# Optimization experiments

Hardware: AMD Instinct MI355X
Metric: run time of the kernel (lower is better)

The kernel has to match this reference:

```python
import jax, jax.numpy as jnp
import numpy as np

B, S, D, H = 4, 2048, 1024, 16
HEAD = D // H
DENOM = float(np.sqrt(D))  # NOTE: original divides by sqrt(hidden_size), not sqrt(head_size)


def setup_inputs() -> dict:
    key = jax.random.key(0)
    ks = jax.random.split(key, 5)
    scale = 1.0 / np.sqrt(D)
    return {
        "hidden_state": jax.random.normal(ks[0], (B, S, D), dtype=jnp.float32),
        "attention_mask": jnp.ones((B, S), dtype=jnp.int32),  # unused in forward (faithful to source)
        "w_q": jax.random.normal(ks[1], (D, D), dtype=jnp.float32) * scale,
        "w_k": jax.random.normal(ks[2], (D, D), dtype=jnp.float32) * scale,
        "w_v": jax.random.normal(ks[3], (D, D), dtype=jnp.float32) * scale,
        "w_o": jax.random.normal(ks[4], (D, D), dtype=jnp.float32) * scale,
    }


def _split_heads(x):
    # [B, S, D] -> [B, H, S, head]
    b, s, _ = x.shape
    return x.reshape(b, s, H, HEAD).transpose(0, 2, 1, 3)


def reference(hidden_state, attention_mask, w_q, w_k, w_v, w_o):
    # nn.Linear(bias=False): y = x @ W^T with W of shape [out, in]
    q = _split_heads(hidden_state @ w_q.T)  # [B, H, S, head]
    k = _split_heads(hidden_state @ w_k.T)
    v = _split_heads(hidden_state @ w_v.T)
    qk = jnp.einsum("bhqd,bhkd->bhqk", q, k) / DENOM  # scale = 1/sqrt(hidden_size)
    attn = jax.nn.softmax(qk, axis=-1)  # attention_mask is NOT applied (matches source)
    ctx = jnp.einsum("bhqk,bhkd->bhqd", attn, v)  # [B, H, S, head]
    ctx = ctx.transpose(0, 2, 1, 3).reshape(hidden_state.shape[0], hidden_state.shape[1], D)
    return ctx @ w_o.T
```

## Files before the change

### kernel.cpp

```cpp
#include <hip/hip_runtime.h>
#include <hip/hip_bf16.h>
#include <math.h>

typedef __bf16 bf16x8 __attribute__((ext_vector_type(8)));
typedef __bf16 bf16x2 __attribute__((ext_vector_type(2)));
typedef float f32x4 __attribute__((ext_vector_type(4)));
typedef float f32x16 __attribute__((ext_vector_type(16)));
typedef unsigned u32x2v __attribute__((ext_vector_type(2)));
typedef unsigned u32x4v __attribute__((ext_vector_type(4)));
typedef unsigned short u16;

#define QSCALE 0.04508422002778011f

__device__ __forceinline__ u16 f2b(float f) {
  union { float f; unsigned u; } x; x.f = f;
  unsigned r = x.u + 0x7fffu + ((x.u >> 16) & 1u);
  return (u16)(r >> 16);
}

__device__ __forceinline__ unsigned pkbf(float a, float b) {
  bf16x2 t = { (__bf16)a, (__bf16)b };
  return __builtin_bit_cast(unsigned, t);
}

#define GLOAD_LDS16(g, s)                                                      \
  __builtin_amdgcn_global_load_lds(                                            \
      (__attribute__((address_space(1))) void*)(void*)(g),                     \
      (__attribute__((address_space(3))) void*)(s), 16, 0, 0)

#define VMCNT4 asm volatile("s_waitcnt vmcnt(4)" ::: "memory")
#define VMCNT0 asm volatile("s_waitcnt vmcnt(0)" ::: "memory")
#define SBAR   __builtin_amdgcn_s_barrier()

__global__ void cast_bf16_kernel(const float* __restrict__ in, u16* __restrict__ out,
                                 int n4) {
  int i = blockIdx.x * blockDim.x + threadIdx.x;
  int stride = gridDim.x * blockDim.x;
  for (; i < n4; i += stride) {
    float4 v = ((const float4*)in)[i];
    ushort4 o;
    o.x = f2b(v.x); o.y = f2b(v.y); o.z = f2b(v.z); o.w = f2b(v.w);
    ((ushort4*)out)[i] = o;
  }
}

__global__ void cast_w4_kernel(const float* __restrict__ wq, const float* __restrict__ wk,
                               const float* __restrict__ wv, const float* __restrict__ wo,
                               u16* __restrict__ wqkv, u16* __restrict__ wob) {
  const int w = blockIdx.y;
  const float* src = (w == 0) ? wq : (w == 1) ? wk : (w == 2) ? wv : wo;
  u16* dst = (w < 3) ? wqkv + (size_t)w * 1024 * 1024 : wob;
  const float scale = (w == 0) ? QSCALE : 1.0f;
  const int n4 = 1024 * 1024 / 4;
  int i = blockIdx.x * blockDim.x + threadIdx.x;
  int stride = gridDim.x * blockDim.x;
  for (; i < n4; i += stride) {
    float4 v = ((const float4*)src)[i];
    ushort4 o;
    o.x = f2b(v.x * scale); o.y = f2b(v.y * scale);
    o.z = f2b(v.z * scale); o.w = f2b(v.w * scale);
    ((ushort4*)dst)[i] = o;
  }
}

template <int OUT_MODE>
__global__ __launch_bounds__(256) void gemm_nt(const u16* __restrict__ A,
                                               const u16* __restrict__ B,
                                               void* __restrict__ O0,
                                               u16* __restrict__ Ko,
                                               u16* __restrict__ Vt) {
  __shared__ u16 As[2][128 * 32];
  __shared__ u16 Bs[2][128 * 32];
  const int tid = threadIdx.x;
  const int wid = tid >> 6, lane = tid & 63;
  const int fr = lane & 15, fg = lane >> 4;
  const int wr = wid >> 1, wc = wid & 1;
  const int m0 = blockIdx.y * 128, n0 = blockIdx.x * 128;
  const int K = 1024;

  const int srow = tid >> 2, skc = tid & 3;
  const int srow2 = (tid + 256) >> 2;

#define STAGE_G(t_) do {                                                             \
    const int d_ = (t_) & 1;                                                         \
    GLOAD_LDS16(A + (size_t)(m0 + srow) * K + (t_) * 32 + skc * 8,                   \
                (char*)As[d_] + tid * 16);                                           \
    GLOAD_LDS16(A + (size_t)(m0 + srow2) * K + (t_) * 32 + skc * 8,                  \
                (char*)As[d_] + (tid + 256) * 16);                                   \
    GLOAD_LDS16(B + (size_t)(n0 + srow) * K + (t_) * 32 + skc * 8,                   \
                (char*)Bs[d_] + tid * 16);                                           \
    GLOAD_LDS16(B + (size_t)(n0 + srow2) * K + (t_) * 32 + skc * 8,                  \
                (char*)Bs[d_] + (tid + 256) * 16);                                   \
  } while (0)

  f32x4 acc[4][4] = {};

  STAGE_G(0);
  for (int t = 0; t < 32; ++t) {
    const int d = t & 1;
    if (t < 31) { STAGE_G(t + 1); VMCNT4; }
    else        { VMCNT0; }
    SBAR;

    bf16x8 af[4], bfr[4];
#pragma unroll
    for (int m = 0; m < 4; ++m)
      af[m] = *(const bf16x8*)((const char*)As[d] + (wr * 64 + m * 16 + fr) * 64 + fg * 16);
#pragma unroll
    for (int n = 0; n < 4; ++n)
      bfr[n] = *(const bf16x8*)((const char*)Bs[d] + (wc * 64 + n * 16 + fr) * 64 + fg * 16);
    __builtin_amdgcn_s_setprio(1);
#pragma unroll
    for (int m = 0; m < 4; ++m)
#pragma unroll
      for (int n = 0; n < 4; ++n)
        acc[m][n] = __builtin_amdgcn_mfma_f32_16x16x32_bf16(af[m], bfr[n], acc[m][n], 0, 0, 0);
    __builtin_amdgcn_s_setprio(0);
    SBAR;
  }
#undef STAGE_G

#pragma unroll
  for (int m = 0; m < 4; ++m)
#pragma unroll
    for (int n = 0; n < 4; ++n) {
      int gr = m0 + wr * 64 + m * 16 + fg * 4;
      int gc = n0 + wc * 64 + n * 16 + fr;
      if (OUT_MODE == 0) {
#pragma unroll
        for (int j = 0; j < 4; ++j)
          ((float*)O0)[(size_t)(gr + j) * 1024 + gc] = acc[m][n][j];
      } else {
        const int region = n0 >> 10;
        if (region == 2) {
          int vc = gc - 2048;
          int hh = vc >> 6, dd = vc & 63, bb2 = gr >> 11, s0 = gr & 2047;
          ushort4 o;
          o.x = f2b(acc[m][n][0]); o.y = f2b(acc[m][n][1]);
          o.z = f2b(acc[m][n][2]); o.w = f2b(acc[m][n][3]);
          *(ushort4*)(Vt + (((size_t)bb2 * 16 + hh) * 64 + dd) * 2048 + s0) = o;
        } else {
          u16* dst = (region == 0) ? (u16*)O0 : Ko;
          int cc = gc & 1023;
#pragma unroll
          for (int j = 0; j < 4; ++j)
            dst[(size_t)(gr + j) * 1024 + cc] = f2b(acc[m][n][j]);
        }
      }
    }
}

__global__ __launch_bounds__(256, 2) void attn_fwd(const u16* __restrict__ Q,
                                                   const u16* __restrict__ Kg,
                                                   const u16* __restrict__ Vtg,
                                                   u16* __restrict__ O) {
  __shared__ u16 Ks[2][64 * 64];
  __shared__ u16 Vs[2][64 * 64];
  const int tid = threadIdx.x;
  const int wid = tid >> 6, lane = tid & 63;
  const int lq = lane & 31, hi = lane >> 5;
  const int id = blockIdx.x;
  const int swz = (id & 7) * 64 + (id >> 3);
  const int qb = swz & 7, bh = swz >> 3;
  const int b = bh >> 4, h = bh & 15;
  const size_t tokBase = (size_t)b * 2048 * 1024 + h * 64;
  const size_t vBase = (size_t)bh * 64 * 2048;
  const int q0 = qb * 256 + wid * 64;

  bf16x8 qfA[4], qfB[4];
#pragma unroll
  for (int s = 0; s < 4; ++s) {
    qfA[s] = *(const bf16x8*)(Q + tokBase + (size_t)(q0 + lq) * 1024 + s * 16 + hi * 8);
    qfB[s] = *(const bf16x8*)(Q + tokBase + (size_t)(q0 + 32 + lq) * 1024 + s * 16 + hi * 8);
  }

  f32x16 accA0 = {}, accA1 = {}, accB0 = {}, accB1 = {};
  f32x16 lsvA = {}, lsvB = {};

  const int skey = tid >> 3, sdc = tid & 7;
  const int sdg = sdc ^ (skey & 7);
  const int skey2 = (tid + 256) >> 3;
  const int sdg2 = sdc ^ (skey2 & 7);

#define STAGE(bb_, k0_) do {                                                          \
    GLOAD_LDS16(Kg + tokBase + (size_t)((k0_) + skey) * 1024 + sdg * 8,               \
                (char*)Ks[bb_] + tid * 16);                                           \
    GLOAD_LDS16(Kg + tokBase + (size_t)((k0_) + skey2) * 1024 + sdg2 * 8,             \
                (char*)Ks[bb_] + (tid + 256) * 16);                                   \
    GLOAD_LDS16(Vtg + vBase + (size_t)skey * 2048 + (k0_) + sdg * 8,                  \
                (char*)Vs[bb_] + tid * 16);                                           \
    GLOAD_LDS16(Vtg + vBase + (size_t)skey2 * 2048 + (k0_) + sdg2 * 8,                \
                (char*)Vs[bb_] + (tid + 256) * 16);                                   \
  } while (0)

  STAGE(0, 0);
  for (int t = 0; t < 32; ++t) {
    const int bb = t & 1;
    __syncthreads();
    if (t < 31) STAGE(bb ^ 1, (t + 1) * 64);

    f32x16 svA0 = {}, svA1 = {}, svB0 = {}, svB1 = {};
    __builtin_amdgcn_s_setprio(1);
#pragma unroll
    for (int s = 0; s < 4; ++s) {
      bf16x8 kf0 = *(const bf16x8*)((const char*)Ks[bb] + lq * 128 +
                                    ((s * 32 + hi * 16) ^ ((lq & 7) << 4)));
      bf16x8 kf1 = *(const bf16x8*)((const char*)Ks[bb] + (32 + lq) * 128 +
                                    ((s * 32 + hi * 16) ^ ((lq & 7) << 4)));
      svA0 = __builtin_amdgcn_mfma_f32_32x32x16_bf16(kf0, qfA[s], svA0, 0, 0, 0);
      svB0 = __builtin_amdgcn_mfma_f32_32x32x16_bf16(kf0, qfB[s], svB0, 0, 0, 0);
      svA1 = __builtin_amdgcn_mfma_f32_32x32x16_bf16(kf1, qfA[s], svA1, 0, 0, 0);
      svB1 = __builtin_amdgcn_mfma_f32_32x32x16_bf16(kf1, qfB[s], svB1, 0, 0, 0);
    }
    __builtin_amdgcn_s_setprio(0);

#pragma unroll
    for (int i = 0; i < 16; ++i) svA0[i] = __builtin_amdgcn_exp2f(svA0[i]);
#pragma unroll
    for (int i = 0; i < 16; ++i) svA1[i] = __builtin_amdgcn_exp2f(svA1[i]);
#pragma unroll
    for (int i = 0; i < 16; ++i) svB0[i] = __builtin_amdgcn_exp2f(svB0[i]);
#pragma unroll
    for (int i = 0; i < 16; ++i) svB1[i] = __builtin_amdgcn_exp2f(svB1[i]);
    lsvA += svA0; lsvA += svA1;
    lsvB += svB0; lsvB += svB1;

    bf16x8 paA[4], paB[4];
#pragma unroll
    for (int kb = 0; kb < 2; ++kb) {
#pragma unroll
      for (int hh = 0; hh < 2; ++hh) {
        const int rb = hh * 8;
        {
          const f32x16& pv = kb ? svA1 : svA0;
          unsigned w01 = pkbf(pv[rb + 0], pv[rb + 1]);
          unsigned w23 = pkbf(pv[rb + 2], pv[rb + 3]);
          unsigned w45 = pkbf(pv[rb + 4], pv[rb + 5]);
          unsigned w67 = pkbf(pv[rb + 6], pv[rb + 7]);
          u32x2v ra = __builtin_amdgcn_permlane32_swap(w01, w45, false, false);
          u32x2v rc = __builtin_amdgcn_permlane32_swap(w23, w67, false, false);
          u32x4v fw = { ra[0], rc[0], ra[1], rc[1] };
          paA[kb * 2 + hh] = __builtin_bit_cast(bf16x8, fw);
        }
        {
          const f32x16& pv = kb ? svB1 : svB0;
          unsigned w01 = pkbf(pv[rb + 0], pv[rb + 1]);
          unsigned w23 = pkbf(pv[rb + 2], pv[rb + 3]);
          unsigned w45 = pkbf(pv[rb + 4], pv[rb + 5]);
          unsigned w67 = pkbf(pv[rb + 6], pv[rb + 7]);
          u32x2v ra = __builtin_amdgcn_permlane32_swap(w01, w45, false, false);
          u32x2v rc = __builtin_amdgcn_permlane32_swap(w23, w67, false, false);
          u32x4v fw = { ra[0], rc[0], ra[1], rc[1] };
          paB[kb * 2 + hh] = __builtin_bit_cast(bf16x8, fw);
        }
      }
    }

    __builtin_amdgcn_s_setprio(1);
#pragma unroll
    for (int s = 0; s < 4; ++s) {
      bf16x8 bv0 = *(const bf16x8*)((const char*)Vs[bb] + lq * 128 +
                                    ((s * 32 + hi * 16) ^ ((lq & 7) << 4)));
      bf16x8 bv1 = *(const bf16x8*)((const char*)Vs[bb] + (32 + lq) * 128 +
                                    ((s * 32 + hi * 16) ^ ((lq & 7) << 4)));
      accA0 = __builtin_amdgcn_mfma_f32_32x32x16_bf16(paA[s], bv0, accA0, 0, 0, 0);
      accA1 = __builtin_amdgcn_mfma_f32_32x32x16_bf16(paA[s], bv1, accA1, 0, 0, 0);
      accB0 = __builtin_amdgcn_mfma_f32_32x32x16_bf16(paB[s], bv0, accB0, 0, 0, 0);
      accB1 = __builtin_amdgcn_mfma_f32_32x32x16_bf16(paB[s], bv1, accB1, 0, 0, 0);
    }
    __builtin_amdgcn_s_setprio(0);
  }
#undef STAGE

  float totA = 0.f, totB = 0.f;
#pragma unroll
  for (int i = 0; i < 16; ++i) { totA += lsvA[i]; totB += lsvB[i]; }
  totA += __shfl_xor(totA, 32);
  totB += __shfl_xor(totB, 32);
  const float invA = 1.0f / totA, invB = 1.0f / totB;
#pragma unroll
  for (int r = 0; r < 16; ++r) {
    const int q = (r & 3) + 8 * (r >> 2) + 4 * hi;
    const float ivA = __shfl(invA, q);
    const float ivB = __shfl(invB, q);
    const size_t rowA = (size_t)(b * 2048 + q0 + q) * 1024 + h * 64;
    const size_t rowB = (size_t)(b * 2048 + q0 + 32 + q) * 1024 + h * 64;
    O[rowA + lq]      = f2b(accA0[r] * ivA);
    O[rowA + 32 + lq] = f2b(accA1[r] * ivA);
    O[rowB + lq]      = f2b(accB0[r] * ivB);
    O[rowB + 32 + lq] = f2b(accB1[r] * ivB);
  }
}

extern "C" void kernel_launch(void* const* d_in, const int* in_sizes, int n_in,
                              void* d_out, int out_size, void* d_ws, size_t ws_size,
                              hipStream_t stream) {
  const float* hs = (const float*)d_in[0];
  const float* wq = (const float*)d_in[2];
  const float* wk = (const float*)d_in[3];
  const float* wv = (const float*)d_in[4];
  const float* wo = (const float*)d_in[5];

  const size_t TOK = 8192, DD = 1024;
  u16* hsb  = (u16*)d_ws;
  u16* wqkv = hsb + TOK * DD;
  u16* wob  = wqkv + 3 * DD * DD;
  u16* Qb   = wob + DD * DD;
  u16* Kb   = Qb + TOK * DD;
  u16* Vtg  = Kb + TOK * DD;
  u16* Cb   = Vtg + TOK * DD;

  cast_bf16_kernel<<<2048, 256, 0, stream>>>(hs, hsb, (int)(TOK * DD / 4));
  cast_w4_kernel<<<dim3(128, 4), 256, 0, stream>>>(wq, wk, wv, wo, wqkv, wob);

  gemm_nt<1><<<dim3(24, 64), 256, 0, stream>>>(hsb, wqkv, Qb, Kb, Vtg);

  attn_fwd<<<dim3(512), 256, 0, stream>>>(Qb, Kb, Vtg, Cb);

  gemm_nt<0><<<dim3(8, 64), 256, 0, stream>>>(Cb, wob, d_out, nullptr, nullptr);
}
```

Before: 206.5 us.

## Use K=64 single-buffered GEMM tiles with XOR-swizzled LDS layout

Rewrites both projection GEMMs to stage 64-wide K slices per iteration instead of 32. LDS writes and reads use an XOR swizzle to avoid bank conflicts. The double-buffered prefetch pipeline is replaced by a single buffer with __syncthreads, which halves the barrier count per K but no longer overlaps global loads with MFMA. This trades load/compute overlap for fewer iterations and conflict-free LDS reads.

```diff
diff --git a/kernel.cpp b/kernel.cpp
--- a/kernel.cpp
+++ b/kernel.cpp
@@ -27,10 +27,6 @@
   __builtin_amdgcn_global_load_lds(                                            \
       (__attribute__((address_space(1))) void*)(void*)(g),                     \
       (__attribute__((address_space(3))) void*)(s), 16, 0, 0)
-
-#define VMCNT4 asm volatile("s_waitcnt vmcnt(4)" ::: "memory")
-#define VMCNT0 asm volatile("s_waitcnt vmcnt(0)" ::: "memory")
-#define SBAR   __builtin_amdgcn_s_barrier()
 
 __global__ void cast_bf16_kernel(const float* __restrict__ in, u16* __restrict__ out,
                                  int n4) {
@@ -64,13 +60,13 @@
 }
 
 template <int OUT_MODE>
-__global__ __launch_bounds__(256) void gemm_nt(const u16* __restrict__ A,
-                                               const u16* __restrict__ B,
-                                               void* __restrict__ O0,
-                                               u16* __restrict__ Ko,
-                                               u16* __restrict__ Vt) {
-  __shared__ u16 As[2][128 * 32];
-  __shared__ u16 Bs[2][128 * 32];
+__global__ __launch_bounds__(256) void gemm_nt64(const u16* __restrict__ A,
+                                                 const u16* __restrict__ B,
+                                                 void* __restrict__ O0,
+                                                 u16* __restrict__ Ko,
+                                                 u16* __restrict__ Vt) {
+  __shared__ u16 As[128 * 64];
+  __shared__ u16 Bs[128 * 64];
   const int tid = threadIdx.x;
   const int wid = tid >> 6, lane = tid & 63;
   const int fr = lane & 15, fg = lane >> 4;
@@ -78,47 +74,48 @@
   const int m0 = blockIdx.y * 128, n0 = blockIdx.x * 128;
   const int K = 1024;
 
-  const int srow = tid >> 2, skc = tid & 3;
-  const int srow2 = (tid + 256) >> 2;
-
-#define STAGE_G(t_) do {                                                             \
-    const int d_ = (t_) & 1;                                                         \
-    GLOAD_LDS16(A + (size_t)(m0 + srow) * K + (t_) * 32 + skc * 8,                   \
-                (char*)As[d_] + tid * 16);                                           \
-    GLOAD_LDS16(A + (size_t)(m0 + srow2) * K + (t_) * 32 + skc * 8,                  \
-                (char*)As[d_] + (tid + 256) * 16);                                   \
-    GLOAD_LDS16(B + (size_t)(n0 + srow) * K + (t_) * 32 + skc * 8,                   \
-                (char*)Bs[d_] + tid * 16);                                           \
-    GLOAD_LDS16(B + (size_t)(n0 + srow2) * K + (t_) * 32 + skc * 8,                  \
-                (char*)Bs[d_] + (tid + 256) * 16);                                   \
-  } while (0)
-
   f32x4 acc[4][4] = {};
 
-  STAGE_G(0);
-  for (int t = 0; t < 32; ++t) {
-    const int d = t & 1;
-    if (t < 31) { STAGE_G(t + 1); VMCNT4; }
-    else        { VMCNT0; }
-    SBAR;
-
-    bf16x8 af[4], bfr[4];
+  for (int kt = 0; kt < K; kt += 64) {
+#pragma unroll
+    for (int i2 = 0; i2 < 4; ++i2) {
+      int c = i2 * 256 + tid;
+      int row = c >> 3, sl = c & 7;
+      int kc = sl ^ (row & 7);
+      GLOAD_LDS16(A + (size_t)(m0 + row) * K + kt + kc * 8, (char*)As + c * 16);
+      GLOAD_LDS16(B + (size_t)(n0 + row) * K + kt + kc * 8, (char*)Bs + c * 16);
+    }
+    __syncthreads();
+
+    bf16x8 af[4][2], bfr[4][2];
+#pragma unroll
+    for (int m = 0; m < 4; ++m) {
+      const int row = wr * 64 + m * 16 + fr;
+#pragma unroll
+      for (int ks = 0; ks < 2; ++ks)
+        af[m][ks] = *(const bf16x8*)((const char*)As + row * 128 +
+                                     ((ks * 64 + fg * 16) ^ ((fr & 7) << 4)));
+    }
+#pragma unroll
+    for (int n = 0; n < 4; ++n) {
+      const int row = wc * 64 + n * 16 + fr;
+#pragma unroll
+      for (int ks = 0; ks < 2; ++ks)
+        bfr[n][ks] = *(const bf16x8*)((const char*)Bs + row * 128 +
+                                      ((ks * 64 + fg * 16) ^ ((fr & 7) << 4)));
+    }
+    __builtin_amdgcn_s_setprio(1);
 #pragma unroll
     for (int m = 0; m < 4; ++m)
-      af[m] = *(const bf16x8*)((const char*)As[d] + (wr * 64 + m * 16 + fr) * 64 + fg * 16);
-#pragma unroll
-    for (int n = 0; n < 4; ++n)
-      bfr[n] = *(const bf16x8*)((const char*)Bs[d] + (wc * 64 + n * 16 + fr) * 64 + fg * 16);
-    __builtin_amdgcn_s_setprio(1);
-#pragma unroll
-    for (int m = 0; m < 4; ++m)
 #pragma unroll
       for (int n = 0; n < 4; ++n)
-        acc[m][n] = __builtin_amdgcn_mfma_f32_16x16x32_bf16(af[m], bfr[n], acc[m][n], 0, 0, 0);
+#pragma unroll
+        for (int ks = 0; ks < 2; ++ks)
+          acc[m][n] = __builtin_amdgcn_mfma_f32_16x16x32_bf16(af[m][ks], bfr[n][ks],
+                                                              acc[m][n], 0, 0, 0);
     __builtin_amdgcn_s_setprio(0);
-    SBAR;
-  }
-#undef STAGE_G
+    __syncthreads();
+  }
 
 #pragma unroll
   for (int m = 0; m < 4; ++m)
@@ -313,9 +310,9 @@
   cast_bf16_kernel<<<2048, 256, 0, stream>>>(hs, hsb, (int)(TOK * DD / 4));
   cast_w4_kernel<<<dim3(128, 4), 256, 0, stream>>>(wq, wk, wv, wo, wqkv, wob);
 
-  gemm_nt<1><<<dim3(24, 64), 256, 0, stream>>>(hsb, wqkv, Qb, Kb, Vtg);
+  gemm_nt64<1><<<dim3(24, 64), 256, 0, stream>>>(hsb, wqkv, Qb, Kb, Vtg);
 
   attn_fwd<<<dim3(512), 256, 0, stream>>>(Qb, Kb, Vtg, Cb);
 
-  gemm_nt<0><<<dim3(8, 64), 256, 0, stream>>>(Cb, wob, d_out, nullptr, nullptr);
-}
+  gemm_nt64<0><<<dim3(8, 64), 256, 0, stream>>>(Cb, wob, d_out, nullptr, nullptr);
+}
```

After: 190.6 us. -7.7%, faster.
